# Performance work log

Measured on AMD Instinct MI355X. Metric: run time of the kernel, lower is better.

## Reference

```python
import jax, jax.numpy as jnp
import numpy as np

H, W = 32, 32
C = 512
HEADS = 8
HEAD_DIM = C // HEADS
B = 8
GROUPS = 32
EPS = 1e-6
N = H * W


def _rel_indices():
    # (N, N) lookup indices into the (2H-1)*(2W-1) relative-position table
    y = np.arange(H)
    x = np.arange(W)
    y1, x1, y2, x2 = np.meshgrid(y, x, y, x, indexing='ij')
    idx = (y1 - y2 + H - 1) * (2 * W - 1) + (x1 - x2 + W - 1)
    return jnp.asarray(idx.reshape(N, N), dtype=jnp.int32)

REL_IDX = _rel_indices()


def setup_inputs() -> dict:
    key = jax.random.key(0)
    ks = jax.random.split(key, 8)
    s = 0.02
    return {
        'x': jax.random.normal(ks[0], (B, C, H, W), jnp.float32),
        '_1': jnp.zeros((1,), jnp.int32),
        '_2': jnp.zeros((1,), jnp.int32),
        'gamma': jnp.ones((C,), jnp.float32),
        'beta': jnp.zeros((C,), jnp.float32),
        'wq': jax.random.normal(ks[1], (C, C), jnp.float32) * s,
        'bq': jnp.zeros((C,), jnp.float32),
        'wk': jax.random.normal(ks[2], (C, C), jnp.float32) * s,
        'bk': jnp.zeros((C,), jnp.float32),
        'wv': jax.random.normal(ks[3], (C, C), jnp.float32) * s,
        'bv': jnp.zeros((C,), jnp.float32),
        'wproj': jax.random.normal(ks[4], (C, C), jnp.float32) * s,
        'bproj': jnp.zeros((C,), jnp.float32),
        'pos_enc': jax.random.normal(ks[5], (HEADS, (2 * H - 1) * (2 * W - 1)), jnp.float32) * s,
    }


def _group_norm(x, gamma, beta):
    b, c, h, w = x.shape
    xg = x.reshape(b, GROUPS, c // GROUPS, h, w)
    mean = xg.mean(axis=(2, 3, 4), keepdims=True)
    var = xg.var(axis=(2, 3, 4), keepdims=True)
    xg = (xg - mean) * jax.lax.rsqrt(var + EPS)
    x = xg.reshape(b, c, h, w)
    return x * gamma[None, :, None, None] + beta[None, :, None, None]


def reference(x, _1, _2, gamma, beta, wq, bq, wk, bk, wv, bv, wproj, bproj, pos_enc):
    x0 = x
    xn = _group_norm(x, gamma, beta)
    xt = xn.reshape(B, C, N)  # (B, C, N)

    def proj(w, bias):
        # 1x1 conv == channel matmul: (B, C_out, N)
        y = jnp.einsum('oc,bcn->bon', w, xt) + bias[None, :, None]
        # split heads: channel index = head*HEAD_DIM + d -> (B, heads, N, d)
        return y.reshape(B, HEADS, HEAD_DIM, N).transpose(0, 1, 3, 2)

    q = proj(wq, bq)
    k = proj(wk, bk)
    v = proj(wv, bv)

    scale = 1.0 / jnp.sqrt(jnp.float32(HEAD_DIM))
    attn = jnp.einsum('bhqd,bhkd->bhqk', q, k) * scale  # (B, heads, N, N)
    rel_bias = pos_enc[:, REL_IDX]  # (heads, N, N)
    attn = attn + rel_bias[None]
    attn = jax.nn.softmax(attn, axis=-1)

    out = jnp.einsum('bhqk,bhkd->bhqd', attn, v)  # (B, heads, N, d)
    out = out.transpose(0, 1, 3, 2).reshape(B, C, H, W)
    out = jnp.einsum('oc,bchw->bohw', wproj, out) + bproj[None, :, None, None]
    return out + x0
```

## Files before the change

kernel.cpp:

```cpp
#include <hip/hip_runtime.h>
#include <hip/hip_bf16.h>
#include <math.h>

typedef __bf16 bf16_t;
typedef __bf16 bf16x8 __attribute__((ext_vector_type(8)));
typedef __bf16 bf16x4 __attribute__((ext_vector_type(4)));
typedef __bf16 bf16x2 __attribute__((ext_vector_type(2)));
typedef float  f32x4  __attribute__((ext_vector_type(4)));
typedef float  f32x16 __attribute__((ext_vector_type(16)));
typedef unsigned u32x4 __attribute__((ext_vector_type(4)));

#define MFMA16(a, b, c) __builtin_amdgcn_mfma_f32_16x16x32_bf16((a), (b), (c), 0, 0, 0)
#define MFMA32(a, b, c) __builtin_amdgcn_mfma_f32_32x32x16_bf16((a), (b), (c), 0, 0, 0)
#define GLDS16(g, s) __builtin_amdgcn_global_load_lds( \
    (const __attribute__((address_space(1))) void*)(g), \
    (__attribute__((address_space(3))) void*)(s), 16, 0, 0)

#define LOG2E 1.4426950408889634f

__global__ __launch_bounds__(256) void cast_weights(
    const float* __restrict__ wq, const float* __restrict__ wk,
    const float* __restrict__ wv, const float* __restrict__ wp,
    bf16_t* __restrict__ Wqkv, bf16_t* __restrict__ Wp)
{
    const int i = (blockIdx.x * 256 + threadIdx.x) * 4;
#pragma unroll
    for (int j = 0; j < 4; ++j) {
        Wqkv[i + j]          = (bf16_t)wq[i + j];
        Wqkv[262144 + i + j] = (bf16_t)wk[i + j];
        Wqkv[524288 + i + j] = (bf16_t)wv[i + j];
        Wp[i + j]            = (bf16_t)wp[i + j];
    }
}

__global__ __launch_bounds__(256) void bias_kernel(
    const float* __restrict__ pos, bf16_t* __restrict__ Bias3)
{
    const int h  = blockIdx.x >> 5;
    const int qt = blockIdx.x & 31;
    const int t = threadIdx.x;
    const int l = t & 63, ko = t >> 6;
    __shared__ bf16_t ps[32][64];

    for (int i = t; i < 32 * 63; i += 256) {
        const int r = i / 63, dx = i - r * 63;
        ps[r][dx] = (bf16_t)(pos[h * 3969 + (qt + r) * 63 + dx] * LOG2E);
    }
    __syncthreads();

    const int qx = l & 31, hi = l >> 5;
#pragma unroll
    for (int kt0 = 0; kt0 < 32; kt0 += 4) {
        const int kt = kt0 + ko;
        const int row = 31 - kt;
        bf16x8 o0, o1;
#pragma unroll
        for (int reg = 0; reg < 16; ++reg) {
            const int kx = (reg & 3) + 8 * (reg >> 2) + 4 * hi;
            const bf16_t v = ps[row][qx - kx + 31];
            if (reg < 8) o0[reg] = v; else o1[reg - 8] = v;
        }
        bf16_t* outp = Bias3 + ((size_t)(((h * 32 + qt) * 32 + kt) * 64 + l)) * 16;
        *(bf16x8*)outp       = o0;
        *(bf16x8*)(outp + 8) = o1;
    }
}

__global__ __launch_bounds__(512) void gn_kernel(
    const float* __restrict__ x, const float* __restrict__ gamma,
    const float* __restrict__ beta, bf16_t* __restrict__ xnT)
{
    const int blk = blockIdx.x;
    const int b = blk >> 5, g = blk & 31;
    const int t = threadIdx.x;
    const int hi = t >> 8, tl = t & 255;
    __shared__ float red[16];
    const float* base = x + ((size_t)b * 512 + g * 16) * 1024;

    f32x4 v[8];
    float s = 0.f, s2 = 0.f;
#pragma unroll
    for (int it = 0; it < 8; ++it) {
        v[it] = *(const f32x4*)(base + (size_t)hi * 8192 + it * 1024 + tl * 4);
#pragma unroll
        for (int j = 0; j < 4; ++j) { s += v[it][j]; s2 += v[it][j] * v[it][j]; }
    }
#pragma unroll
    for (int m = 1; m < 64; m <<= 1) { s += __shfl_xor(s, m); s2 += __shfl_xor(s2, m); }
    const int w = t >> 6;
    if ((t & 63) == 0) { red[w] = s; red[8 + w] = s2; }
    __syncthreads();
    s = 0.f; s2 = 0.f;
#pragma unroll
    for (int i = 0; i < 8; ++i) { s += red[i]; s2 += red[8 + i]; }
    const float mean = s * (1.f / 16384.f);
    const float var  = fmaxf(s2 * (1.f / 16384.f) - mean * mean, 0.f);
    const float rstd = rsqrtf(var + 1e-6f);

    float ga[8], be[8];
#pragma unroll
    for (int it = 0; it < 8; ++it) {
        const int gc = g * 16 + hi * 8 + it;
        ga[it] = gamma[gc] * rstd;
        be[it] = beta[gc] - mean * ga[it];
    }
#pragma unroll
    for (int j = 0; j < 4; ++j) {
        bf16x8 o;
#pragma unroll
        for (int it = 0; it < 8; ++it)
            o[it] = (bf16_t)(v[it][j] * ga[it] + be[it]);
        *(bf16x8*)(xnT + ((size_t)b * 1024 + tl * 4 + j) * 512 + g * 16 + hi * 8) = o;
    }
}

__global__ __launch_bounds__(256) void gemm_bt(
    const bf16_t* __restrict__ A, const bf16_t* __restrict__ Bt, int mode,
    int mtiles,
    const float* __restrict__ bias0, const float* __restrict__ bias1,
    const float* __restrict__ bias2,
    const float* __restrict__ x0, float* __restrict__ outF,
    bf16_t* __restrict__ Qb, bf16_t* __restrict__ Kb, bf16_t* __restrict__ Vb)
{
    const int K  = 512;
    const int g  = blockIdx.x;
    const int xcd = g & 7;
    const int i_  = g >> 3;
    const int m_idx = i_ % mtiles;
    const int n_idx = xcd * 8 + i_ / mtiles;
    const int m0 = m_idx * 128;
    const int n0 = n_idx * 128;
    const int t = threadIdx.x;
    const int l = t & 63, w = t >> 6;
    const int wr = w >> 1, wc = w & 1;
    const int lrow = l & 15, lgrp = l >> 4;

    __shared__ __align__(16) char smem_raw[49152];
    bf16_t* Ct = (bf16_t*)smem_raw;

    f32x4 acc[4][4];
#pragma unroll
    for (int i = 0; i < 4; ++i)
#pragma unroll
        for (int j = 0; j < 4; ++j) acc[i][j] = (f32x4){0.f, 0.f, 0.f, 0.f};

    const bf16_t* gA0 = A  + (size_t)(m0 + w * 16 + (l >> 2)) * K + (l & 3) * 8;
    const bf16_t* gA1 = gA0 + (size_t)64 * K;
    const bf16_t* gB0 = Bt + (size_t)(n0 + w * 16 + (l >> 2)) * K + (l & 3) * 8;
    const bf16_t* gB1 = gB0 + (size_t)64 * K;

#define STAGE(s, k0) do {                                                   \
    bf16_t* As_ = (bf16_t*)(smem_raw + (s) * 16384);                        \
    bf16_t* Bs_ = (bf16_t*)(smem_raw + (s) * 16384 + 8192);                 \
    GLDS16(gA0 + (k0), As_ + w * 512);                                      \
    GLDS16(gA1 + (k0), As_ + 2048 + w * 512);                               \
    GLDS16(gB0 + (k0), Bs_ + w * 512);                                      \
    GLDS16(gB1 + (k0), Bs_ + 2048 + w * 512); } while (0)

    STAGE(0, 0);
    STAGE(1, 32);

#pragma unroll
    for (int tk = 0; tk < 16; ++tk) {
        if (tk < 15) asm volatile("s_waitcnt vmcnt(4)" ::: "memory");
        else         asm volatile("s_waitcnt vmcnt(0)" ::: "memory");
        __builtin_amdgcn_s_barrier();
        __builtin_amdgcn_sched_barrier(0);
        if (tk + 2 < 16) STAGE((tk + 2) % 3, (tk + 2) * 32);
        const bf16_t* Asb = (const bf16_t*)(smem_raw + (tk % 3) * 16384);
        const bf16_t* Bsb = Asb + 4096;
        bf16x8 af[4], bfr[4];
#pragma unroll
        for (int ms = 0; ms < 4; ++ms)
            af[ms] = *(const bf16x8*)&Asb[(wr * 64 + ms * 16 + lrow) * 32 + lgrp * 8];
#pragma unroll
        for (int ns = 0; ns < 4; ++ns)
            bfr[ns] = *(const bf16x8*)&Bsb[(wc * 64 + ns * 16 + lrow) * 32 + lgrp * 8];
        __builtin_amdgcn_s_setprio(1);
#pragma unroll
        for (int ms = 0; ms < 4; ++ms)
#pragma unroll
            for (int ns = 0; ns < 4; ++ns)
                acc[ms][ns] = MFMA16(af[ms], bfr[ns], acc[ms][ns]);
        __builtin_amdgcn_s_setprio(0);
    }
#undef STAGE

    if (mode == 0) {
        const int which = m0 >> 9;
        const int mq = (m0 >> 7) & 3;
        const float* bias = (which == 0) ? bias0 : (which == 1) ? bias1 : bias2;
        const float scl = (which == 0) ? 0.125f * LOG2E : 1.0f;
        const int b   = n_idx >> 3;
        const int nn0 = (n_idx & 7) * 128;

        __syncthreads();
        if (which < 2) {
            bf16_t* Qk = (which == 0) ? Qb : Kb;
#pragma unroll
            for (int ms = 0; ms < 4; ++ms) {
                const int ml = wr * 64 + ms * 16 + lgrp * 4;
#pragma unroll
                for (int ns = 0; ns < 4; ++ns) {
                    const int nl = wc * 64 + ns * 16 + lrow;
                    bf16x4 pk;
#pragma unroll
                    for (int j = 0; j < 4; ++j)
                        pk[j] = (bf16_t)((acc[ms][ns][j] + bias[mq * 128 + ml + j]) * scl);
                    *(bf16x4*)&Ct[nl * 136 + ml] = pk;
                }
            }
            __syncthreads();
#pragma unroll
            for (int it = 0; it < 8; ++it) {
                const int idx = it * 256 + t;
                const int token = idx >> 4, oc = idx & 15;
                const bf16x8 vv8 = *(const bf16x8*)&Ct[token * 136 + oc * 8];
                const int head = mq * 2 + (oc >> 3);
                const int d = (oc & 7) * 8;
                *(bf16x8*)(Qk + (((size_t)b * 8 + head) * 1024 + nn0 + token) * 64 + d) = vv8;
            }
        } else {
#pragma unroll
            for (int ms = 0; ms < 4; ++ms) {
                const int ml = wr * 64 + ms * 16 + lgrp * 4;
#pragma unroll
                for (int ns = 0; ns < 4; ++ns) {
                    const int nl = wc * 64 + ns * 16 + lrow;
#pragma unroll
                    for (int j = 0; j < 4; ++j)
                        Ct[(ml + j) * 136 + nl] =
                            (bf16_t)(acc[ms][ns][j] + bias[mq * 128 + ml + j]);
                }
            }
            __syncthreads();
#pragma unroll
            for (int it = 0; it < 8; ++it) {
                const int idx = it * 256 + t;
                const int o = idx >> 4, nc = idx & 15;
                const bf16x8 vv8 = *(const bf16x8*)&Ct[o * 136 + nc * 8];
                const int head = mq * 2 + (o >> 6);
                const int d = o & 63;
                *(bf16x8*)(Vb + (((size_t)b * 8 + head) * 64 + d) * 1024 + nn0 + nc * 8) = vv8;
            }
        }
    } else {
#pragma unroll
        for (int ms = 0; ms < 4; ++ms) {
#pragma unroll
            for (int ns = 0; ns < 4; ++ns) {
                const int c  = m0 + wr * 64 + ms * 16 + lgrp * 4;
                const int np = n0 + wc * 64 + ns * 16 + lrow;
                const int b = np >> 10, n = np & 1023;
#pragma unroll
                for (int j = 0; j < 4; ++j) {
                    const size_t idx = ((size_t)b * 512 + c + j) * 1024 + n;
                    outF[idx] = acc[ms][ns][j] + bias0[c + j] + x0[idx];
                }
            }
        }
    }
}

__global__ __launch_bounds__(512, 2) void attn_kernel(
    const bf16_t* __restrict__ Qb, const bf16_t* __restrict__ Kb,
    const bf16_t* __restrict__ Vb, const bf16_t* __restrict__ Bias3,
    bf16_t* __restrict__ Xo)
{
    const int bh = blockIdx.x;
    const int h  = bh & 7;
    const int q0 = blockIdx.y * 256;
    const int t = threadIdx.x;
    const int w = t >> 6, l = t & 63;
    const int lq = l & 31, hi = l >> 5;

    __shared__ __align__(16) bf16_t Ks[128][72];
    __shared__ __align__(16) bf16_t Vs[64][136];

    const int qrow = q0 + w * 32 + lq;
    const bf16_t* qbase = Qb + ((size_t)bh * 1024 + qrow) * 64;
    bf16x8 qf[4];
#pragma unroll
    for (int dc = 0; dc < 4; ++dc)
        qf[dc] = *(const bf16x8*)(qbase + dc * 16 + hi * 8);

    const bf16_t* bbase = Bias3 +
        ((size_t)((h * 32 + (q0 >> 5) + w) * 32)) * 1024 + (size_t)l * 16;

    bf16x8 ones;
#pragma unroll
    for (int i = 0; i < 8; ++i) ones[i] = (bf16_t)1.0f;

    f32x16 oacc[2], tsacc;
#pragma unroll
    for (int j = 0; j < 16; ++j) { oacc[0][j] = 0.f; oacc[1][j] = 0.f; tsacc[j] = 0.f; }

    const int sr2 = t >> 3;
    const int sc2 = (t & 7) * 8;
    const bf16_t* Kg = Kb + ((size_t)bh * 1024 + sr2) * 64 + sc2;
    const bf16_t* Vg = Vb + ((size_t)bh * 64 + sr2) * 1024 + sc2;

    bf16x8 kv0 = *(const bf16x8*)(Kg);
    bf16x8 kv1 = *(const bf16x8*)(Kg + (size_t)64 * 64);
    bf16x8 vv0 = *(const bf16x8*)(Vg);
    bf16x8 vv1 = *(const bf16x8*)(Vg + 64);
    bf16x8 bA[8], bB[8];
#pragma unroll
    for (int k = 0; k < 4; ++k) {
        bA[2 * k]     = *(const bf16x8*)(bbase + (size_t)k * 1024);
        bA[2 * k + 1] = *(const bf16x8*)(bbase + (size_t)k * 1024 + 8);
    }

    auto dtile = [&](int it, bf16x8 (&bcur)[8], bf16x8 (&bnxt)[8]) {
        const int nk0 = it * 128;
        __syncthreads();
        *(bf16x8*)&Ks[sr2][sc2]      = kv0;
        *(bf16x8*)&Ks[64 + sr2][sc2] = kv1;
        *(bf16x8*)&Vs[sr2][sc2]      = vv0;
        *(bf16x8*)&Vs[sr2][64 + sc2] = vv1;
        __syncthreads();
        if (it < 7) {
            const int nkn = nk0 + 128;
#pragma unroll
            for (int k = 0; k < 4; ++k) {
                bnxt[2 * k]     = *(const bf16x8*)(bbase + (size_t)((it + 1) * 4 + k) * 1024);
                bnxt[2 * k + 1] = *(const bf16x8*)(bbase + (size_t)((it + 1) * 4 + k) * 1024 + 8);
            }
            kv0 = *(const bf16x8*)(Kg + (size_t)nkn * 64);
            kv1 = *(const bf16x8*)(Kg + (size_t)(nkn + 64) * 64);
            vv0 = *(const bf16x8*)(Vg + nkn);
            vv1 = *(const bf16x8*)(Vg + nkn + 64);
        }

#pragma unroll
        for (int kt = 0; kt < 4; ++kt) {
            const int ktloc = kt * 32;
            f32x16 sa;
#pragma unroll
            for (int r = 0; r < 8; ++r) {
                sa[r]     = (float)bcur[2 * kt][r];
                sa[8 + r] = (float)bcur[2 * kt + 1][r];
            }
#pragma unroll
            for (int dc = 0; dc < 4; ++dc) {
                const bf16x8 kf = *(const bf16x8*)&Ks[ktloc + lq][dc * 16 + hi * 8];
                sa = MFMA32(kf, qf[dc], sa);
            }
            unsigned W00, W01, W10, W11, W20, W21, W30, W31;
            {
                float p[16];
#pragma unroll
                for (int r = 0; r < 16; ++r) p[r] = exp2f(sa[r]);
                bf16x2 tw;
#define PACKW(dst, a, b_) { tw[0] = (bf16_t)p[a]; tw[1] = (bf16_t)p[b_]; \
                            dst = __builtin_bit_cast(unsigned, tw); }
                PACKW(W00, 0, 1)   PACKW(W01, 2, 3)
                PACKW(W10, 4, 5)   PACKW(W11, 6, 7)
                PACKW(W20, 8, 9)   PACKW(W21, 10, 11)
                PACKW(W30, 12, 13) PACKW(W31, 14, 15)
#undef PACKW
            }
            asm volatile("v_permlane32_swap_b32 %0, %1" : "+v"(W00), "+v"(W10));
            asm volatile("v_permlane32_swap_b32 %0, %1" : "+v"(W01), "+v"(W11));
            asm volatile("v_permlane32_swap_b32 %0, %1" : "+v"(W20), "+v"(W30));
            asm volatile("v_permlane32_swap_b32 %0, %1" : "+v"(W21), "+v"(W31));
            const bf16x8 pf0 = __builtin_bit_cast(bf16x8, (u32x4){W00, W01, W10, W11});
            const bf16x8 pf1 = __builtin_bit_cast(bf16x8, (u32x4){W20, W21, W30, W31});

            tsacc = MFMA32(ones, pf0, tsacc);
            tsacc = MFMA32(ones, pf1, tsacc);
#pragma unroll
            for (int dh = 0; dh < 2; ++dh) {
                const bf16x8 vf0 = *(const bf16x8*)&Vs[dh * 32 + lq][ktloc + hi * 8];
                const bf16x8 vf1 = *(const bf16x8*)&Vs[dh * 32 + lq][ktloc + 16 + hi * 8];
                oacc[dh] = MFMA32(vf0, pf0, oacc[dh]);
                oacc[dh] = MFMA32(vf1, pf1, oacc[dh]);
            }
        }
    };

    for (int it2 = 0; it2 < 8; it2 += 2) {
        dtile(it2,     bA, bB);
        dtile(it2 + 1, bB, bA);
    }

    const float inv = 1.0f / tsacc[0];

    const int b = bh >> 3;
    const int q = q0 + w * 32 + lq;
    bf16_t* xrow = Xo + ((size_t)b * 1024 + q) * 512 + h * 64;
#pragma unroll
    for (int dh = 0; dh < 2; ++dh)
#pragma unroll
        for (int rr = 0; rr < 4; ++rr) {
            bf16x4 o4;
#pragma unroll
            for (int j = 0; j < 4; ++j)
                o4[j] = (bf16_t)(oacc[dh][4 * rr + j] * inv);
            *(bf16x4*)(xrow + dh * 32 + 8 * rr + 4 * hi) = o4;
        }
}

extern "C" void kernel_launch(void* const* d_in, const int* in_sizes, int n_in,
                              void* d_out, int out_size, void* d_ws, size_t ws_size,
                              hipStream_t stream)
{
    const float* x     = (const float*)d_in[0];
    const float* gamma = (const float*)d_in[3];
    const float* beta  = (const float*)d_in[4];
    const float* wq    = (const float*)d_in[5];
    const float* bq    = (const float*)d_in[6];
    const float* wk    = (const float*)d_in[7];
    const float* bk    = (const float*)d_in[8];
    const float* wv    = (const float*)d_in[9];
    const float* bv    = (const float*)d_in[10];
    const float* wp    = (const float*)d_in[11];
    const float* bp    = (const float*)d_in[12];
    const float* pos   = (const float*)d_in[13];
    float* out = (float*)d_out;

    size_t off = 0;
    char* wsb = (char*)d_ws;
    auto alloc = [&](size_t bytes) { char* p = wsb + off; off += bytes; return p; };
    bf16_t* Wqkv  = (bf16_t*)alloc((size_t)1536 * 512 * 2);
    bf16_t* Wp    = (bf16_t*)alloc((size_t)512 * 512 * 2);
    bf16_t* xnT   = (bf16_t*)alloc((size_t)8192 * 512 * 2);
    bf16_t* Qb    = (bf16_t*)alloc((size_t)8192 * 512 * 2);
    bf16_t* Kb    = (bf16_t*)alloc((size_t)8192 * 512 * 2);
    bf16_t* Vb    = (bf16_t*)alloc((size_t)8192 * 512 * 2);
    bf16_t* Xo    = (bf16_t*)alloc((size_t)8192 * 512 * 2);
    bf16_t* Bias3 = (bf16_t*)alloc((size_t)8 * 32 * 32 * 64 * 16 * 2);

    hipLaunchKernelGGL(cast_weights, dim3(256), dim3(256), 0, stream,
                       wq, wk, wv, wp, Wqkv, Wp);
    hipLaunchKernelGGL(bias_kernel, dim3(256), dim3(256), 0, stream, pos, Bias3);
    hipLaunchKernelGGL(gn_kernel, dim3(256), dim3(512), 0, stream,
                       x, gamma, beta, xnT);
    hipLaunchKernelGGL(gemm_bt, dim3(768), dim3(256), 0, stream,
                       Wqkv, xnT, 0, 12, bq, bk, bv,
                       nullptr, nullptr, Qb, Kb, Vb);
    hipLaunchKernelGGL(attn_kernel, dim3(64, 4), dim3(512), 0, stream,
                       Qb, Kb, Vb, Bias3, Xo);
    hipLaunchKernelGGL(gemm_bt, dim3(256), dim3(256), 0, stream,
                       Wp, Xo, 1, 4, bp, nullptr, nullptr,
                       x, out, nullptr, nullptr, nullptr);
}
```

Measured before the change: 93.19 us.

## Split attention key tiles across wave halves and combine partial outputs in shared memory

```diff
diff --git a/kernel.cpp b/kernel.cpp
--- a/kernel.cpp
+++ b/kernel.cpp
@@ -262,22 +262,25 @@
     }
 }
 
-__global__ __launch_bounds__(512, 2) void attn_kernel(
+__global__ __launch_bounds__(512, 4) void attn_kernel(
     const bf16_t* __restrict__ Qb, const bf16_t* __restrict__ Kb,
     const bf16_t* __restrict__ Vb, const bf16_t* __restrict__ Bias3,
     bf16_t* __restrict__ Xo)
 {
     const int bh = blockIdx.x;
     const int h  = bh & 7;
-    const int q0 = blockIdx.y * 256;
+    const int q0 = blockIdx.y * 128;
     const int t = threadIdx.x;
     const int w = t >> 6, l = t & 63;
+    const int qc = w & 3, half = w >> 2;
     const int lq = l & 31, hi = l >> 5;
 
-    __shared__ __align__(16) bf16_t Ks[128][72];
-    __shared__ __align__(16) bf16_t Vs[64][136];
-
-    const int qrow = q0 + w * 32 + lq;
+    __shared__ __align__(16) char smem[35840];
+    bf16_t* Ks = (bf16_t*)smem;
+    bf16_t* Vs = (bf16_t*)(smem + 18432);
+    float*  comb = (float*)smem;
+
+    const int qrow = q0 + qc * 32 + lq;
     const bf16_t* qbase = Qb + ((size_t)bh * 1024 + qrow) * 64;
     bf16x8 qf[4];
 #pragma unroll
@@ -285,7 +288,7 @@
         qf[dc] = *(const bf16x8*)(qbase + dc * 16 + hi * 8);
 
     const bf16_t* bbase = Bias3 +
-        ((size_t)((h * 32 + (q0 >> 5) + w) * 32)) * 1024 + (size_t)l * 16;
+        ((size_t)((h * 32 + (q0 >> 5) + qc) * 32)) * 1024 + (size_t)l * 16;
 
     bf16x8 ones;
 #pragma unroll
@@ -304,27 +307,28 @@
     bf16x8 kv1 = *(const bf16x8*)(Kg + (size_t)64 * 64);
     bf16x8 vv0 = *(const bf16x8*)(Vg);
     bf16x8 vv1 = *(const bf16x8*)(Vg + 64);
-    bf16x8 bA[8], bB[8];
-#pragma unroll
-    for (int k = 0; k < 4; ++k) {
-        bA[2 * k]     = *(const bf16x8*)(bbase + (size_t)k * 1024);
-        bA[2 * k + 1] = *(const bf16x8*)(bbase + (size_t)k * 1024 + 8);
-    }
-
-    auto dtile = [&](int it, bf16x8 (&bcur)[8], bf16x8 (&bnxt)[8]) {
+    bf16x8 bA[4], bB[4];
+#pragma unroll
+    for (int k = 0; k < 2; ++k) {
+        bA[2 * k]     = *(const bf16x8*)(bbase + (size_t)(half * 2 + k) * 1024);
+        bA[2 * k + 1] = *(const bf16x8*)(bbase + (size_t)(half * 2 + k) * 1024 + 8);
+    }
+
+    auto dtile = [&](int it, bf16x8 (&bcur)[4], bf16x8 (&bnxt)[4]) {
         const int nk0 = it * 128;
         __syncthreads();
-        *(bf16x8*)&Ks[sr2][sc2]      = kv0;
-        *(bf16x8*)&Ks[64 + sr2][sc2] = kv1;
-        *(bf16x8*)&Vs[sr2][sc2]      = vv0;
-        *(bf16x8*)&Vs[sr2][64 + sc2] = vv1;
+        *(bf16x8*)&Ks[(sr2) * 72 + sc2]      = kv0;
+        *(bf16x8*)&Ks[(64 + sr2) * 72 + sc2] = kv1;
+        *(bf16x8*)&Vs[sr2 * 136 + sc2]       = vv0;
+        *(bf16x8*)&Vs[sr2 * 136 + 64 + sc2]  = vv1;
         __syncthreads();
         if (it < 7) {
             const int nkn = nk0 + 128;
 #pragma unroll
-            for (int k = 0; k < 4; ++k) {
-                bnxt[2 * k]     = *(const bf16x8*)(bbase + (size_t)((it + 1) * 4 + k) * 1024);
-                bnxt[2 * k + 1] = *(const bf16x8*)(bbase + (size_t)((it + 1) * 4 + k) * 1024 + 8);
+            for (int k = 0; k < 2; ++k) {
+                const size_t tkn = (size_t)((it + 1) * 4 + half * 2 + k) * 1024;
+                bnxt[2 * k]     = *(const bf16x8*)(bbase + tkn);
+                bnxt[2 * k + 1] = *(const bf16x8*)(bbase + tkn + 8);
             }
             kv0 = *(const bf16x8*)(Kg + (size_t)nkn * 64);
             kv1 = *(const bf16x8*)(Kg + (size_t)(nkn + 64) * 64);
@@ -333,17 +337,17 @@
         }
 
 #pragma unroll
-        for (int kt = 0; kt < 4; ++kt) {
-            const int ktloc = kt * 32;
+        for (int ktl = 0; ktl < 2; ++ktl) {
+            const int ktloc = half * 64 + ktl * 32;
             f32x16 sa;
 #pragma unroll
             for (int r = 0; r < 8; ++r) {
-                sa[r]     = (float)bcur[2 * kt][r];
-                sa[8 + r] = (float)bcur[2 * kt + 1][r];
+                sa[r]     = (float)bcur[2 * ktl][r];
+                sa[8 + r] = (float)bcur[2 * ktl + 1][r];
             }
 #pragma unroll
             for (int dc = 0; dc < 4; ++dc) {
-                const bf16x8 kf = *(const bf16x8*)&Ks[ktloc + lq][dc * 16 + hi * 8];
+                const bf16x8 kf = *(const bf16x8*)&Ks[(ktloc + lq) * 72 + dc * 16 + hi * 8];
                 sa = MFMA32(kf, qf[dc], sa);
             }
             unsigned W00, W01, W10, W11, W20, W21, W30, W31;
@@ -371,8 +375,8 @@
             tsacc = MFMA32(ones, pf1, tsacc);
 #pragma unroll
             for (int dh = 0; dh < 2; ++dh) {
-                const bf16x8 vf0 = *(const bf16x8*)&Vs[dh * 32 + lq][ktloc + hi * 8];
-                const bf16x8 vf1 = *(const bf16x8*)&Vs[dh * 32 + lq][ktloc + 16 + hi * 8];
+                const bf16x8 vf0 = *(const bf16x8*)&Vs[(dh * 32 + lq) * 136 + ktloc + hi * 8];
+                const bf16x8 vf1 = *(const bf16x8*)&Vs[(dh * 32 + lq) * 136 + ktloc + 16 + hi * 8];
                 oacc[dh] = MFMA32(vf0, pf0, oacc[dh]);
                 oacc[dh] = MFMA32(vf1, pf1, oacc[dh]);
             }
@@ -384,21 +388,34 @@
         dtile(it2 + 1, bB, bA);
     }
 
-    const float inv = 1.0f / tsacc[0];
-
-    const int b = bh >> 3;
-    const int q = q0 + w * 32 + lq;
-    bf16_t* xrow = Xo + ((size_t)b * 1024 + q) * 512 + h * 64;
-#pragma unroll
-    for (int dh = 0; dh < 2; ++dh)
-#pragma unroll
-        for (int rr = 0; rr < 4; ++rr) {
-            bf16x4 o4;
-#pragma unroll
-            for (int j = 0; j < 4; ++j)
-                o4[j] = (bf16_t)(oacc[dh][4 * rr + j] * inv);
-            *(bf16x4*)(xrow + dh * 32 + 8 * rr + 4 * hi) = o4;
-        }
+    __syncthreads();
+    if (half == 1) {
+        float* p = comb + ((size_t)qc * 64 + l) * 33;
+#pragma unroll
+        for (int j = 0; j < 16; ++j) { p[j] = oacc[0][j]; p[16 + j] = oacc[1][j]; }
+        p[32] = tsacc[0];
+    }
+    __syncthreads();
+    if (half == 0) {
+        const float* p = comb + ((size_t)qc * 64 + l) * 33;
+#pragma unroll
+        for (int j = 0; j < 16; ++j) { oacc[0][j] += p[j]; oacc[1][j] += p[16 + j]; }
+        const float inv = 1.0f / (tsacc[0] + p[32]);
+
+        const int b = bh >> 3;
+        const int q = q0 + qc * 32 + lq;
+        bf16_t* xrow = Xo + ((size_t)b * 1024 + q) * 512 + h * 64;
+#pragma unroll
+        for (int dh = 0; dh < 2; ++dh)
+#pragma unroll
+            for (int rr = 0; rr < 4; ++rr) {
+                bf16x4 o4;
+#pragma unroll
+                for (int j = 0; j < 4; ++j)
+                    o4[j] = (bf16_t)(oacc[dh][4 * rr + j] * inv);
+                *(bf16x4*)(xrow + dh * 32 + 8 * rr + 4 * hi) = o4;
+            }
+    }
 }
 
 extern "C" void kernel_launch(void* const* d_in, const int* in_sizes, int n_in,
@@ -439,7 +456,7 @@
     hipLaunchKernelGGL(gemm_bt, dim3(768), dim3(256), 0, stream,
                        Wqkv, xnT, 0, 12, bq, bk, bv,
                        nullptr, nullptr, Qb, Kb, Vb);
-    hipLaunchKernelGGL(attn_kernel, dim3(64, 4), dim3(512), 0, stream,
+    hipLaunchKernelGGL(attn_kernel, dim3(64, 8), dim3(512), 0, stream,
                        Qb, Kb, Vb, Bias3, Xo);
     hipLaunchKernelGGL(gemm_bt, dim3(256), dim3(256), 0, stream,
                        Wp, Xo, 1, 4, bp, nullptr, nullptr,
```

Result: slower. 135.0 us (+44.8%).
